# Performance work log

Hardware: AMD Instinct MI355X
Metric: run time of the kernel (lower is better)

The kernel has to match this reference:

```python
import jax, jax.numpy as jnp
import numpy as np

N_HEADS = 16
HEAD_DIM = 128
ROPE_BASE = 10000.0


def _apply_rope(x, start_pos):
    # x: [B, T, H, Dh]; interleaved-pair RoPE (llama-style)
    B, T, H, Dh = x.shape
    half = Dh // 2
    inv_freq = 1.0 / (ROPE_BASE ** (jnp.arange(0, Dh, 2, dtype=jnp.float32) / Dh))  # [half]
    pos = jnp.arange(T, dtype=jnp.float32) + start_pos                              # [T]
    ang = pos[:, None] * inv_freq[None, :]                                          # [T, half]
    cos = jnp.cos(ang)[None, :, None, :].astype(x.dtype)                            # [1,T,1,half]
    sin = jnp.sin(ang)[None, :, None, :].astype(x.dtype)
    x1 = x[..., 0::2]
    x2 = x[..., 1::2]
    r1 = x1 * cos - x2 * sin
    r2 = x1 * sin + x2 * cos
    return jnp.stack([r1, r2], axis=-1).reshape(B, T, H, Dh)


def setup_inputs() -> dict:
    key = jax.random.key(0)
    k0, k1, k2, k3, k4 = jax.random.split(key, 5)
    B, T, D = 2, 2048, 2048
    d_lat = 1024
    x = jax.random.normal(k0, (B, T, D), dtype=jnp.float32)
    wq = jax.random.normal(k1, (D, N_HEADS * HEAD_DIM), dtype=jnp.float32) / np.sqrt(D)
    w_down = jax.random.normal(k2, (D, d_lat), dtype=jnp.float32) / np.sqrt(D)
    w_up = jax.random.normal(k3, (d_lat, 2 * N_HEADS * HEAD_DIM), dtype=jnp.float32) / np.sqrt(d_lat)
    wo = jax.random.normal(k4, (N_HEADS * HEAD_DIM, D), dtype=jnp.float32) / np.sqrt(N_HEADS * HEAD_DIM)
    return {"x": x, "wq": wq, "w_down": w_down, "w_up": w_up, "wo": wo}


def reference(x, wq, w_down, w_up, wo):
    # Prefill path: use_cache=False, mask=None -> causal, start_pos=0, n_kv_heads==n_heads
    B, T, D = x.shape
    H, Dh = N_HEADS, HEAD_DIM
    scale = Dh ** -0.5

    q = (x @ wq).reshape(B, T, H, Dh)
    c_kv = x @ w_down                               # [B, T, d_latent]
    kv_up = (c_kv @ w_up).reshape(B, T, H, 2 * Dh)  # latent decompression
    k, v = kv_up[..., :Dh], kv_up[..., Dh:]

    q = _apply_rope(q, 0)
    k = _apply_rope(k, 0)

    scores = jnp.einsum('bqhd,bkhd->bhqk', q, k) * scale  # [B,H,T,T]
    causal = jnp.tril(jnp.ones((T, T), dtype=bool))
    scores = jnp.where(causal[None, None, :, :], scores, jnp.float32(-jnp.inf))
    attn = jax.nn.softmax(scores, axis=-1)
    out = jnp.einsum('bhqk,bkhd->bqhd', attn, v).reshape(B, T, H * Dh)
    return out @ wo
```

## Files before the change

### kernel.cpp

```cpp
#include <hip/hip_runtime.h>
#include <math.h>
#include <stdint.h>

#define T_SEQ 2048
#define DMODEL 2048
#define DLAT 1024
#define NH 16
#define DH 128
#define BATCH 2
#define MTOT (BATCH * T_SEQ)

typedef float f32x4 __attribute__((ext_vector_type(4)));
typedef __bf16 bf16x8 __attribute__((ext_vector_type(8)));

__device__ __forceinline__ unsigned short f2bf(float f) {
    return __builtin_bit_cast(unsigned short, (__bf16)f);
}

#define EXP2F(x) __builtin_amdgcn_exp2f(x)

__device__ __forceinline__ float red16_max(float v) {
    int x = __builtin_bit_cast(int, v);
    v = fmaxf(v, __builtin_bit_cast(float, __builtin_amdgcn_update_dpp(x, x, 0xB1, 0xf, 0xf, false)));
    x = __builtin_bit_cast(int, v);
    v = fmaxf(v, __builtin_bit_cast(float, __builtin_amdgcn_update_dpp(x, x, 0x4E, 0xf, 0xf, false)));
    x = __builtin_bit_cast(int, v);
    v = fmaxf(v, __builtin_bit_cast(float, __builtin_amdgcn_update_dpp(x, x, 0x124, 0xf, 0xf, false)));
    x = __builtin_bit_cast(int, v);
    v = fmaxf(v, __builtin_bit_cast(float, __builtin_amdgcn_update_dpp(x, x, 0x128, 0xf, 0xf, false)));
    return v;
}
__device__ __forceinline__ float red16_sum(float v) {
    int x = __builtin_bit_cast(int, v);
    v += __builtin_bit_cast(float, __builtin_amdgcn_update_dpp(x, x, 0xB1, 0xf, 0xf, false));
    x = __builtin_bit_cast(int, v);
    v += __builtin_bit_cast(float, __builtin_amdgcn_update_dpp(x, x, 0x4E, 0xf, 0xf, false));
    x = __builtin_bit_cast(int, v);
    v += __builtin_bit_cast(float, __builtin_amdgcn_update_dpp(x, x, 0x124, 0xf, 0xf, false));
    x = __builtin_bit_cast(int, v);
    v += __builtin_bit_cast(float, __builtin_amdgcn_update_dpp(x, x, 0x128, 0xf, 0xf, false));
    return v;
}

#define GLL16(g, l) __builtin_amdgcn_global_load_lds( \
    (const __attribute__((address_space(1))) unsigned int*)(g), \
    (__attribute__((address_space(3))) unsigned int*)(l), 16, 0, 0)

__global__ void rope_table_kernel(float* __restrict__ cosb, float* __restrict__ sinb) {
    int idx = blockIdx.x * blockDim.x + threadIdx.x;
    if (idx >= T_SEQ * 64) return;
    int t = idx >> 6;
    int i = idx & 63;
    float inv = expf(-((2.0f * (float)i) / 128.0f) * logf(10000.0f));
    float ang = (float)t * inv;
    cosb[idx] = cosf(ang);
    sinb[idx] = sinf(ang);
}

__global__ void conv_f2b_kernel(const float* __restrict__ s, unsigned short* __restrict__ d) {
    int i = (blockIdx.x * blockDim.x + threadIdx.x) * 4;
    float4 v = *(const float4*)(s + i);
    ushort4 o;
    o.x = f2bf(v.x); o.y = f2bf(v.y); o.z = f2bf(v.z); o.w = f2bf(v.w);
    *(ushort4*)(d + i) = o;
}

__global__ void transpose_f2b_kernel(const float* __restrict__ src, unsigned short* __restrict__ dst,
                                     int R, int C) {
    __shared__ unsigned short tile[32][33];
    int tx = threadIdx.x & 31, ty = threadIdx.x >> 5;
    int r0 = blockIdx.y * 32, c0 = blockIdx.x * 32;
#pragma unroll
    for (int i = 0; i < 32; i += 8)
        tile[ty + i][tx] = f2bf(src[(size_t)(r0 + ty + i) * C + c0 + tx]);
    __syncthreads();
#pragma unroll
    for (int i = 0; i < 32; i += 8)
        dst[(size_t)(c0 + ty + i) * R + r0 + tx] = tile[tx][ty + i];
}

__global__ void transpose_b2b_kernel(const unsigned short* __restrict__ src, unsigned short* __restrict__ dst,
                                     int R, int C) {
    __shared__ unsigned short tile[32][33];
    int tx = threadIdx.x & 31, ty = threadIdx.x >> 5;
    int r0 = blockIdx.y * 32, c0 = blockIdx.x * 32;
#pragma unroll
    for (int i = 0; i < 32; i += 8)
        tile[ty + i][tx] = src[(size_t)(r0 + ty + i) * C + c0 + tx];
    __syncthreads();
#pragma unroll
    for (int i = 0; i < 32; i += 8)
        dst[(size_t)(c0 + ty + i) * R + r0 + tx] = tile[tx][ty + i];
}

template <int EPI>
__global__ __launch_bounds__(256)
void gemm_bf16_kernel(const unsigned short* __restrict__ A, const unsigned short* __restrict__ BT,
                      void* __restrict__ C0, void* __restrict__ C1,
                      const float* __restrict__ cosb, const float* __restrict__ sinb,
                      int M, int N, int K) {
    __shared__ unsigned short As[128 * 32];
    __shared__ unsigned short Bs[128 * 32];
    const int t = threadIdx.x;
    const int w = t >> 6, l = t & 63;
    const int wr = w >> 1, wc = w & 1;
    const int lr = l & 15, lg = l >> 4;
    const int m0 = blockIdx.y * 128, n0 = blockIdx.x * 128;

    f32x4 acc[4][4] = {{}};

    const unsigned short* aP  = A  + (size_t)(m0 + (t >> 2)) * K + (t & 3) * 8;
    const unsigned short* aP2 = aP + (size_t)64 * K;
    const unsigned short* bP  = BT + (size_t)(n0 + (t >> 2)) * K + (t & 3) * 8;
    const unsigned short* bP2 = bP + (size_t)64 * K;

    for (int k0 = 0; k0 < K; k0 += 32) {
        __syncthreads();
        GLL16(aP  + k0, &As[t * 8]);
        GLL16(aP2 + k0, &As[2048 + t * 8]);
        GLL16(bP  + k0, &Bs[t * 8]);
        GLL16(bP2 + k0, &Bs[2048 + t * 8]);
        __syncthreads();

        bf16x8 af[4], bfr[4];
#pragma unroll
        for (int i = 0; i < 4; ++i)
            af[i] = *(const bf16x8*)&As[(wr * 64 + i * 16 + lr) * 32 + lg * 8];
#pragma unroll
        for (int j = 0; j < 4; ++j)
            bfr[j] = *(const bf16x8*)&Bs[(wc * 64 + j * 16 + lr) * 32 + lg * 8];
#pragma unroll
        for (int i = 0; i < 4; ++i)
#pragma unroll
            for (int j = 0; j < 4; ++j)
                acc[i][j] = __builtin_amdgcn_mfma_f32_16x16x32_bf16(af[i], bfr[j], acc[i][j], 0, 0, 0);
    }

    const bool is_v  = (EPI == 2) && ((n0 & 128) != 0);
    const bool is_cv = (EPI == 4) && (n0 >= 2048);
#pragma unroll
    for (int i = 0; i < 4; ++i) {
#pragma unroll
        for (int j = 0; j < 4; ++j) {
#pragma unroll
            for (int rr = 0; rr < 4; ++rr) {
                const int row_g = m0 + wr * 64 + i * 16 + lg * 4 + rr;
                const int col_g = n0 + wc * 64 + j * 16 + lr;
                float v = acc[i][j][rr];
                if (EPI == 2) {
                    float res = v;
                    if (!is_v) {
                        float o_ = __shfl_xor(v, 1);
                        int d = col_g & 127;
                        int tp = row_g & (T_SEQ - 1);
                        float c = cosb[tp * 64 + (d >> 1)];
                        float s = sinb[tp * 64 + (d >> 1)];
                        res = (lr & 1) ? (o_ * s + v * c) : (v * c - o_ * s);
                    }
                    int dcol = ((col_g >> 8) << 7) | (col_g & 127);
                    unsigned short* dst = is_v ? (unsigned short*)C1 : (unsigned short*)C0;
                    dst[(size_t)row_g * DMODEL + dcol] = f2bf(res);
                } else if (EPI == 3) {
                    ((float*)C0)[(size_t)row_g * N + col_g] = v;
                } else {
                    if (!is_cv) {
                        float o_ = __shfl_xor(v, 1);
                        int d = col_g & 127;
                        int tp = row_g & (T_SEQ - 1);
                        float c = cosb[tp * 64 + (d >> 1)];
                        float s = sinb[tp * 64 + (d >> 1)];
                        float res = (lr & 1) ? (o_ * s + v * c) : (v * c - o_ * s);
                        ((unsigned short*)C0)[(size_t)row_g * DMODEL + col_g] = f2bf(res);
                    } else {
                        ((unsigned short*)C1)[(size_t)row_g * DLAT + (col_g - 2048)] = f2bf(v);
                    }
                }
            }
        }
    }
}

__global__ __launch_bounds__(256, 2)
void attn_mfma2_kernel(const unsigned short* __restrict__ qb, const unsigned short* __restrict__ kb,
                       const unsigned short* __restrict__ vT, unsigned short* __restrict__ ob) {
    __shared__ __align__(16) unsigned short Ks[2][64 * 128];
    __shared__ __align__(16) unsigned short Vs[128 * 64];
    __shared__ __align__(16) unsigned short Ps[4][16][64];

    const int bh = blockIdx.x;
    const int b = bh >> 4, h = bh & 15;
    const int qt = 15 - blockIdx.y;
    const int t = threadIdx.x;
    const int w = t >> 6, l = t & 63;
    const int lr = l & 15, lg = l >> 4;

    const unsigned short* kbase = kb + (size_t)(b * T_SEQ) * DMODEL + h * DH;
    const unsigned short* vbase = vT + (size_t)(h * DH) * MTOT + (size_t)b * T_SEQ;
    const float sc2 = 0.08838834764831845f * 1.44269504089f;

    const int q0 = qt * 128;
    const int q_base = q0 + w * 32;

    bf16x8 qf[2][4];
#pragma unroll
    for (int rg = 0; rg < 2; ++rg) {
        const unsigned short* qrow = qb + (size_t)(b * T_SEQ + q_base + rg * 16 + lr) * DMODEL + h * DH;
#pragma unroll
        for (int c = 0; c < 4; ++c) qf[rg][c] = *(const bf16x8*)(qrow + c * 32 + lg * 8);
    }

    f32x4 o[2][8] = {{}};
    float m[2][4], lsum[2][4];
#pragma unroll
    for (int rg = 0; rg < 2; ++rg)
#pragma unroll
        for (int r = 0; r < 4; ++r) { m[rg][r] = -3.0e38f; lsum[rg][r] = 0.f; }

    const int nt = 2 * qt + 2;
    int cur = 0;

#pragma unroll
    for (int i = 0; i < 4; ++i) {
        int c = i * 256 + t;
        int row = c >> 4;
        int k16 = (c & 15) ^ (row & 7);
        GLL16(kbase + (size_t)row * DMODEL + k16 * 8, &Ks[0][c * 8]);
    }
    __syncthreads();

    for (int kt = 0; kt < nt; ++kt) {
        const int k0 = kt * 64;
        if (kt + 1 < nt) {
            const int kn = k0 + 64;
#pragma unroll
            for (int i = 0; i < 4; ++i) {
                int c = i * 256 + t;
                int row = c >> 4;
                int k16 = (c & 15) ^ (row & 7);
                GLL16(kbase + (size_t)(kn + row) * DMODEL + k16 * 8, &Ks[cur ^ 1][c * 8]);
            }
        }
#pragma unroll
        for (int i = 0; i < 4; ++i) {
            int c = i * 256 + t;
            int d = c >> 3;
            int k8 = (c & 7) ^ (d & 7);
            GLL16(vbase + (size_t)d * MTOT + k0 + k8 * 8, &Vs[c * 8]);
        }

        f32x4 s[2][4] = {{}};
        __builtin_amdgcn_s_setprio(1);
#pragma unroll
        for (int j = 0; j < 4; ++j) {
            const int krow = j * 16 + lr;
#pragma unroll
            for (int c = 0; c < 4; ++c) {
                bf16x8 kf = *(const bf16x8*)&Ks[cur][krow * 128 + (((c * 4 + lg) ^ (krow & 7)) * 8)];
                s[0][j] = __builtin_amdgcn_mfma_f32_16x16x32_bf16(qf[0][c], kf, s[0][j], 0, 0, 0);
                s[1][j] = __builtin_amdgcn_mfma_f32_16x16x32_bf16(qf[1][c], kf, s[1][j], 0, 0, 0);
            }
        }
        __builtin_amdgcn_s_setprio(0);

#pragma unroll
        for (int rg = 0; rg < 2; ++rg) {
            const int qb0 = q_base + rg * 16;
#pragma unroll
            for (int j = 0; j < 4; ++j)
#pragma unroll
                for (int r = 0; r < 4; ++r) s[rg][j][r] *= sc2;
            if (k0 + 63 > qb0) {
#pragma unroll
                for (int j = 0; j < 4; ++j) {
                    const int key = k0 + j * 16 + lr;
#pragma unroll
                    for (int r = 0; r < 4; ++r)
                        if (key > qb0 + lg * 4 + r) s[rg][j][r] = -3.0e38f;
                }
            }
            float tm[4];
            int need = 0;
#pragma unroll
            for (int r = 0; r < 4; ++r) {
                float v = fmaxf(fmaxf(s[rg][0][r], s[rg][1][r]), fmaxf(s[rg][2][r], s[rg][3][r]));
                tm[r] = red16_max(v);
                need |= (tm[r] - m[rg][r] > 8.0f) ? 1 : 0;
            }
            if (__any(need)) {
#pragma unroll
                for (int r = 0; r < 4; ++r) {
                    const float mn = fmaxf(m[rg][r], tm[r]);
                    const float a = EXP2F(m[rg][r] - mn);
                    m[rg][r] = mn;
                    lsum[rg][r] *= a;
#pragma unroll
                    for (int i = 0; i < 8; ++i) o[rg][i][r] *= a;
                }
            }
#pragma unroll
            for (int r = 0; r < 4; ++r) {
                float rs = 0.f;
#pragma unroll
                for (int j = 0; j < 4; ++j) { s[rg][j][r] = EXP2F(s[rg][j][r] - m[rg][r]); rs += s[rg][j][r]; }
                lsum[rg][r] += red16_sum(rs);
            }
        }

        __syncthreads();

        bf16x8 pa[2][2];
#pragma unroll
        for (int rg = 0; rg < 2; ++rg) {
#pragma unroll
            for (int j = 0; j < 4; ++j) {
#pragma unroll
                for (int r = 0; r < 4; ++r) {
                    const int prow = lg * 4 + r;
                    const int chunk = (j * 2 + (lr >> 3)) ^ (prow & 7);
                    Ps[w][prow][chunk * 8 + (lr & 7)] = f2bf(s[rg][j][r]);
                }
            }
#pragma unroll
            for (int kc = 0; kc < 2; ++kc)
                pa[rg][kc] = *(const bf16x8*)&Ps[w][lr][((kc * 4 + lg) ^ (lr & 7)) * 8];
        }

        __builtin_amdgcn_s_setprio(1);
#pragma unroll
        for (int i = 0; i < 8; ++i) {
            const int d = i * 16 + lr;
#pragma unroll
            for (int kc = 0; kc < 2; ++kc) {
                bf16x8 vf = *(const bf16x8*)&Vs[d * 64 + (((kc * 4 + lg) ^ (d & 7)) * 8)];
                o[0][i] = __builtin_amdgcn_mfma_f32_16x16x32_bf16(pa[0][kc], vf, o[0][i], 0, 0, 0);
                o[1][i] = __builtin_amdgcn_mfma_f32_16x16x32_bf16(pa[1][kc], vf, o[1][i], 0, 0, 0);
            }
        }
        __builtin_amdgcn_s_setprio(0);
        __syncthreads();
        cur ^= 1;
    }

#pragma unroll
    for (int rg = 0; rg < 2; ++rg) {
        float inv[4];
#pragma unroll
        for (int r = 0; r < 4; ++r) inv[r] = 1.f / lsum[rg][r];
#pragma unroll
        for (int i = 0; i < 8; ++i)
#pragma unroll
            for (int r = 0; r < 4; ++r)
                ob[(size_t)(b * T_SEQ + q_base + rg * 16 + lg * 4 + r) * DMODEL + h * DH + i * 16 + lr]
                    = f2bf(o[rg][i][r] * inv[r]);
    }
}

extern "C" void kernel_launch(void* const* d_in, const int* in_sizes, int n_in,
                              void* d_out, int out_size, void* d_ws, size_t ws_size,
                              hipStream_t stream) {
    const float* x      = (const float*)d_in[0];
    const float* wq     = (const float*)d_in[1];
    const float* w_down = (const float*)d_in[2];
    const float* w_up   = (const float*)d_in[3];
    const float* wo     = (const float*)d_in[4];
    float* out = (float*)d_out;

    uint8_t* p = (uint8_t*)d_ws;
    float* cosb = (float*)p;            p += (size_t)T_SEQ * 64 * 4;
    float* sinb = (float*)p;            p += (size_t)T_SEQ * 64 * 4;
    unsigned short* xb   = (unsigned short*)p; p += (size_t)MTOT * DMODEL * 2;
    unsigned short* wqT  = (unsigned short*)p; p += (size_t)DMODEL * DMODEL * 2;
    unsigned short* wdT  = (unsigned short*)p; p += (size_t)DLAT * DMODEL * 2;
    unsigned short* wuT  = (unsigned short*)p; p += (size_t)(2 * NH * DH) * DLAT * 2;
    unsigned short* woT  = (unsigned short*)p; p += (size_t)DMODEL * DMODEL * 2;
    unsigned short* qbuf = (unsigned short*)p; p += (size_t)MTOT * DMODEL * 2;
    unsigned short* ckv  = (unsigned short*)p; p += (size_t)MTOT * DLAT * 2;
    unsigned short* kbuf = (unsigned short*)p; p += (size_t)MTOT * DMODEL * 2;
    unsigned short* vbuf = (unsigned short*)p; p += (size_t)MTOT * DMODEL * 2;
    unsigned short* vT   = (unsigned short*)p; p += (size_t)DMODEL * MTOT * 2;
    unsigned short* abuf = xb;

    rope_table_kernel<<<(T_SEQ * 64) / 256, 256, 0, stream>>>(cosb, sinb);
    conv_f2b_kernel<<<(MTOT * DMODEL / 4) / 256, 256, 0, stream>>>(x, xb);
    transpose_f2b_kernel<<<dim3(DMODEL / 32, DMODEL / 32), 256, 0, stream>>>(wq, wqT, DMODEL, DMODEL);
    transpose_f2b_kernel<<<dim3(DLAT / 32, DMODEL / 32), 256, 0, stream>>>(w_down, wdT, DMODEL, DLAT);
    transpose_f2b_kernel<<<dim3((2 * NH * DH) / 32, DLAT / 32), 256, 0, stream>>>(w_up, wuT, DLAT, 2 * NH * DH);
    transpose_f2b_kernel<<<dim3(DMODEL / 32, DMODEL / 32), 256, 0, stream>>>(wo, woT, DMODEL, DMODEL);

    gemm_bf16_kernel<4><<<dim3((DMODEL + DLAT) / 128, MTOT / 128), 256, 0, stream>>>(
        xb, wqT, qbuf, ckv, cosb, sinb, MTOT, DMODEL + DLAT, DMODEL);
    gemm_bf16_kernel<2><<<dim3((2 * NH * DH) / 128, MTOT / 128), 256, 0, stream>>>(
        ckv, wuT, kbuf, vbuf, cosb, sinb, MTOT, 2 * NH * DH, DLAT);
    transpose_b2b_kernel<<<dim3(DMODEL / 32, MTOT / 32), 256, 0, stream>>>(vbuf, vT, MTOT, DMODEL);
    attn_mfma2_kernel<<<dim3(BATCH * NH, 16), 256, 0, stream>>>(qbuf, kbuf, vT, abuf);
    gemm_bf16_kernel<3><<<dim3(DMODEL / 128, MTOT / 128), 256, 0, stream>>>(
        abuf, woT, out, nullptr, cosb, sinb, MTOT, DMODEL, DMODEL);
}
```

Baseline: 451.9 us.

## Single-buffer attention K tile for higher occupancy, fold softmax scale, merge transposes

The attention kernel drops K double-buffering, which halves the K shared-memory footprint, and raises launch bounds to 4 blocks per CU. The aim is to hide latency through occupancy rather than software prefetch. The attention scale times log2(e) is folded into the Q RoPE epilogue of the first GEMM, which removes a per-score multiply in the attention loop. The four weight transpose launches are merged into one kernel to cut launch overhead. Risks are exposed K/V load latency, since the loads are now synchronous each iteration, possible register spilling under the tighter bound, and bf16 rounding of the pre-scaled Q.

```diff
diff --git a/kernel.cpp b/kernel.cpp
--- a/kernel.cpp
+++ b/kernel.cpp
@@ -65,18 +65,29 @@
     *(ushort4*)(d + i) = o;
 }
 
-__global__ void transpose_f2b_kernel(const float* __restrict__ src, unsigned short* __restrict__ dst,
-                                     int R, int C) {
-    __shared__ unsigned short tile[32][33];
-    int tx = threadIdx.x & 31, ty = threadIdx.x >> 5;
-    int r0 = blockIdx.y * 32, c0 = blockIdx.x * 32;
+__global__ __launch_bounds__(256)
+void transpose_all_kernel(const float* __restrict__ wq, const float* __restrict__ wdn,
+                          const float* __restrict__ wup, const float* __restrict__ wo,
+                          unsigned short* __restrict__ wqT, unsigned short* __restrict__ wdT,
+                          unsigned short* __restrict__ wuT, unsigned short* __restrict__ woT) {
+    const int tile = blockIdx.x;
+    const float* src; unsigned short* dst; int R, C, local;
+    if (tile < 4096)       { src = wq;  dst = wqT; R = 2048; C = 2048; local = tile; }
+    else if (tile < 6144)  { src = wdn; dst = wdT; R = 2048; C = 1024; local = tile - 4096; }
+    else if (tile < 10240) { src = wup; dst = wuT; R = 1024; C = 4096; local = tile - 6144; }
+    else                   { src = wo;  dst = woT; R = 2048; C = 2048; local = tile - 10240; }
+    const int ctiles = C >> 5;
+    const int c0 = (local & (ctiles - 1)) * 32;
+    const int r0 = (local / ctiles) * 32;
+    __shared__ unsigned short t16[32][33];
+    const int tx = threadIdx.x & 31, ty = threadIdx.x >> 5;
 #pragma unroll
     for (int i = 0; i < 32; i += 8)
-        tile[ty + i][tx] = f2bf(src[(size_t)(r0 + ty + i) * C + c0 + tx]);
+        t16[ty + i][tx] = f2bf(src[(size_t)(r0 + ty + i) * C + c0 + tx]);
     __syncthreads();
 #pragma unroll
     for (int i = 0; i < 32; i += 8)
-        dst[(size_t)(c0 + ty + i) * R + r0 + tx] = tile[tx][ty + i];
+        dst[(size_t)(c0 + ty + i) * R + r0 + tx] = t16[tx][ty + i];
 }
 
 __global__ void transpose_b2b_kernel(const unsigned short* __restrict__ src, unsigned short* __restrict__ dst,
@@ -136,6 +147,7 @@
                 acc[i][j] = __builtin_amdgcn_mfma_f32_16x16x32_bf16(af[i], bfr[j], acc[i][j], 0, 0, 0);
     }
 
+    const float SC2 = 0.08838834764831845f * 1.44269504089f;
     const bool is_v  = (EPI == 2) && ((n0 & 128) != 0);
     const bool is_cv = (EPI == 4) && (n0 >= 2048);
 #pragma unroll
@@ -170,7 +182,7 @@
                         float c = cosb[tp * 64 + (d >> 1)];
                         float s = sinb[tp * 64 + (d >> 1)];
                         float res = (lr & 1) ? (o_ * s + v * c) : (v * c - o_ * s);
-                        ((unsigned short*)C0)[(size_t)row_g * DMODEL + col_g] = f2bf(res);
+                        ((unsigned short*)C0)[(size_t)row_g * DMODEL + col_g] = f2bf(res * SC2);
                     } else {
                         ((unsigned short*)C1)[(size_t)row_g * DLAT + (col_g - 2048)] = f2bf(v);
                     }
@@ -180,10 +192,10 @@
     }
 }
 
-__global__ __launch_bounds__(256, 2)
+__global__ __launch_bounds__(256, 4)
 void attn_mfma2_kernel(const unsigned short* __restrict__ qb, const unsigned short* __restrict__ kb,
                        const unsigned short* __restrict__ vT, unsigned short* __restrict__ ob) {
-    __shared__ __align__(16) unsigned short Ks[2][64 * 128];
+    __shared__ __align__(16) unsigned short Ks[64 * 128];
     __shared__ __align__(16) unsigned short Vs[128 * 64];
     __shared__ __align__(16) unsigned short Ps[4][16][64];
 
@@ -196,7 +208,6 @@
 
     const unsigned short* kbase = kb + (size_t)(b * T_SEQ) * DMODEL + h * DH;
     const unsigned short* vbase = vT + (size_t)(h * DH) * MTOT + (size_t)b * T_SEQ;
-    const float sc2 = 0.08838834764831845f * 1.44269504089f;
 
     const int q0 = qt * 128;
     const int q_base = q0 + w * 32;
@@ -217,28 +228,16 @@
         for (int r = 0; r < 4; ++r) { m[rg][r] = -3.0e38f; lsum[rg][r] = 0.f; }
 
     const int nt = 2 * qt + 2;
-    int cur = 0;
-
-#pragma unroll
-    for (int i = 0; i < 4; ++i) {
-        int c = i * 256 + t;
-        int row = c >> 4;
-        int k16 = (c & 15) ^ (row & 7);
-        GLL16(kbase + (size_t)row * DMODEL + k16 * 8, &Ks[0][c * 8]);
-    }
-    __syncthreads();
 
     for (int kt = 0; kt < nt; ++kt) {
         const int k0 = kt * 64;
-        if (kt + 1 < nt) {
-            const int kn = k0 + 64;
-#pragma unroll
-            for (int i = 0; i < 4; ++i) {
-                int c = i * 256 + t;
-                int row = c >> 4;
-                int k16 = (c & 15) ^ (row & 7);
-                GLL16(kbase + (size_t)(kn + row) * DMODEL + k16 * 8, &Ks[cur ^ 1][c * 8]);
-            }
+        __syncthreads();
+#pragma unroll
+        for (int i = 0; i < 4; ++i) {
+            int c = i * 256 + t;
+            int row = c >> 4;
+            int k16 = (c & 15) ^ (row & 7);
+            GLL16(kbase + (size_t)(k0 + row) * DMODEL + k16 * 8, &Ks[c * 8]);
         }
 #pragma unroll
         for (int i = 0; i < 4; ++i) {
@@ -247,6 +246,7 @@
             int k8 = (c & 7) ^ (d & 7);
             GLL16(vbase + (size_t)d * MTOT + k0 + k8 * 8, &Vs[c * 8]);
         }
+        __syncthreads();
 
         f32x4 s[2][4] = {{}};
         __builtin_amdgcn_s_setprio(1);
@@ -255,7 +255,7 @@
             const int krow = j * 16 + lr;
 #pragma unroll
             for (int c = 0; c < 4; ++c) {
-                bf16x8 kf = *(const bf16x8*)&Ks[cur][krow * 128 + (((c * 4 + lg) ^ (krow & 7)) * 8)];
+                bf16x8 kf = *(const bf16x8*)&Ks[krow * 128 + (((c * 4 + lg) ^ (krow & 7)) * 8)];
                 s[0][j] = __builtin_amdgcn_mfma_f32_16x16x32_bf16(qf[0][c], kf, s[0][j], 0, 0, 0);
                 s[1][j] = __builtin_amdgcn_mfma_f32_16x16x32_bf16(qf[1][c], kf, s[1][j], 0, 0, 0);
             }
@@ -265,10 +265,6 @@
 #pragma unroll
         for (int rg = 0; rg < 2; ++rg) {
             const int qb0 = q_base + rg * 16;
-#pragma unroll
-            for (int j = 0; j < 4; ++j)
-#pragma unroll
-                for (int r = 0; r < 4; ++r) s[rg][j][r] *= sc2;
             if (k0 + 63 > qb0) {
 #pragma unroll
                 for (int j = 0; j < 4; ++j) {
@@ -306,8 +302,6 @@
             }
         }
 
-        __syncthreads();
-
         bf16x8 pa[2][2];
 #pragma unroll
         for (int rg = 0; rg < 2; ++rg) {
@@ -337,8 +331,6 @@
             }
         }
         __builtin_amdgcn_s_setprio(0);
-        __syncthreads();
-        cur ^= 1;
     }
 
 #pragma unroll
@@ -382,10 +374,7 @@
 
     rope_table_kernel<<<(T_SEQ * 64) / 256, 256, 0, stream>>>(cosb, sinb);
     conv_f2b_kernel<<<(MTOT * DMODEL / 4) / 256, 256, 0, stream>>>(x, xb);
-    transpose_f2b_kernel<<<dim3(DMODEL / 32, DMODEL / 32), 256, 0, stream>>>(wq, wqT, DMODEL, DMODEL);
-    transpose_f2b_kernel<<<dim3(DLAT / 32, DMODEL / 32), 256, 0, stream>>>(w_down, wdT, DMODEL, DLAT);
-    transpose_f2b_kernel<<<dim3((2 * NH * DH) / 32, DLAT / 32), 256, 0, stream>>>(w_up, wuT, DLAT, 2 * NH * DH);
-    transpose_f2b_kernel<<<dim3(DMODEL / 32, DMODEL / 32), 256, 0, stream>>>(wo, woT, DMODEL, DMODEL);
+    transpose_all_kernel<<<14336, 256, 0, stream>>>(wq, w_down, w_up, wo, wqT, wdT, wuT, woT);
 
     gemm_bf16_kernel<4><<<dim3((DMODEL + DLAT) / 128, MTOT / 128), 256, 0, stream>>>(
         xb, wqT, qbuf, ckv, cosb, sinb, MTOT, DMODEL + DLAT, DMODEL);
```

New measurement: 686.9 us. +52.0%, slower.
